# Kernel tuning notes

Hardware: AMD Instinct MI355X
Metric: run time of the kernel (lower is better)

## Reference

```python
import jax, jax.numpy as jnp
import numpy as np

B, N, DIM = 4, 2048, 1024
H, DH = 16, 64
SCALE = DH ** -0.5


def setup_inputs() -> dict:
    key = jax.random.key(0)
    k1, k2, k3, k4 = jax.random.split(key, 4)
    x = jax.random.normal(k1, (B, N, DIM), dtype=jnp.float32)
    mask = jax.random.randint(k2, (B, N, N), 0, 2, dtype=jnp.int32)
    W_qkv = jax.random.normal(k3, (DIM, 3 * H * DH), dtype=jnp.float32) * (DIM ** -0.5)
    W_out = jax.random.normal(k4, (H * DH, DIM), dtype=jnp.float32) * ((H * DH) ** -0.5)
    b_out = jnp.zeros((DIM,), dtype=jnp.float32)
    return {"x": x, "mask": mask, "W_qkv": W_qkv, "W_out": W_out, "b_out": b_out}


def reference(x, mask, W_qkv, W_out, b_out):
    # QKV projection: [b, n, 3*h*d]
    qkv = x @ W_qkv
    q, k, v = jnp.split(qkv, 3, axis=-1)
    # 'b n (h d) -> b h n d'
    def to_heads(t):
        b, n, _ = t.shape
        return t.reshape(b, n, H, DH).transpose(0, 2, 1, 3)
    q, k, v = to_heads(q), to_heads(k), to_heads(v)
    # scaled dot-product scores: [b, h, n, n]
    scores = jnp.einsum('bhnd,bhmd->bhnm', q, k) * SCALE
    scores = jnp.where(mask[:, None, :, :] == 1, -jnp.inf, scores)
    att = jax.nn.softmax(scores, axis=-1)
    out = jnp.einsum('bhnm,bhmd->bhnd', att, v)
    # 'b h n d -> b n (h d)'
    out = out.transpose(0, 2, 1, 3).reshape(x.shape[0], x.shape[1], H * DH)
    return out @ W_out + b_out
```

## Files before the change

kernel.cpp:

```cpp
#include <hip/hip_runtime.h>
#include <hip/hip_bf16.h>


typedef __attribute__((ext_vector_type(8))) short bf16x8;
typedef __attribute__((ext_vector_type(4))) float f32x4;

__device__ __forceinline__ unsigned short f2bf(float f) {
  unsigned u = __builtin_bit_cast(unsigned, f);
  u += 0x7fffu + ((u >> 16) & 1u);
  return (unsigned short)(u >> 16);
}

__device__ __forceinline__ void gload16(const void* g, void* l) {
  __builtin_amdgcn_global_load_lds(
      (const __attribute__((address_space(1))) unsigned int*)g,
      (__attribute__((address_space(3))) unsigned int*)l, 16, 0, 0);
}

__device__ __forceinline__ bf16x8 ldsw(const short* base, int row, int elem) {
  const char* p = (const char*)base + row * 128 + ((elem * 2) ^ ((row & 7) << 4));
  return *(const bf16x8*)p;
}

__global__ __launch_bounds__(256) void k_cvt(const float* __restrict__ in,
                                             unsigned short* __restrict__ out) {
  int i = (blockIdx.x * 256 + threadIdx.x) * 4;
  float4 v = *reinterpret_cast<const float4*>(in + i);
  ushort4 o;
  o.x = f2bf(v.x); o.y = f2bf(v.y); o.z = f2bf(v.z); o.w = f2bf(v.w);
  *reinterpret_cast<ushort4*>(out + i) = o;
}

__global__ __launch_bounds__(256) void k_transpose_cvt(const float* __restrict__ in,
                                                       unsigned short* __restrict__ out,
                                                       int rows, int cols) {
  __shared__ float tile[32][33];
  int tx = threadIdx.x & 31, ty = threadIdx.x >> 5;
  int c0 = blockIdx.x * 32, r0 = blockIdx.y * 32;
#pragma unroll
  for (int i = 0; i < 32; i += 8)
    tile[ty + i][tx] = in[(size_t)(r0 + ty + i) * cols + (c0 + tx)];
  __syncthreads();
#pragma unroll
  for (int i = 0; i < 32; i += 8)
    out[(size_t)(c0 + ty + i) * rows + (r0 + tx)] = f2bf(tile[tx][ty + i]);
}

__global__ __launch_bounds__(256) void k_packmask(const int* __restrict__ mask,
                                                  unsigned long long* __restrict__ pack) {
  const int row = blockIdx.x;
  const int t = threadIdx.x, w = t >> 6, lane = t & 63;
  const int* mrow = mask + (size_t)row * 2048;
#pragma unroll
  for (int it = 0; it < 8; ++it) {
    int key = it * 256 + w * 64 + lane;
    unsigned long long bal = __ballot(mrow[key] == 1);
    if (lane == 0) pack[(size_t)row * 32 + it * 4 + w] = bal;
  }
}

template <int EPI>
__global__ __launch_bounds__(256) void k_gemm(
    const unsigned short* __restrict__ A, const unsigned short* __restrict__ Bt,
    unsigned short* __restrict__ Qo, unsigned short* __restrict__ Ko,
    unsigned short* __restrict__ Vo, float* __restrict__ Co,
    const float* __restrict__ bias) {
  __shared__ __align__(16) short As[128 * 64];
  __shared__ __align__(16) short Bs[128 * 64];
  const int t = threadIdx.x;
  const int bn = blockIdx.x, bm = blockIdx.y;
  const int wid = t >> 6, lane = t & 63, g = lane >> 4, l15 = lane & 15;
  const int wr = wid >> 1, wc = wid & 1;
  f32x4 zero = {0.f, 0.f, 0.f, 0.f};
  f32x4 acc[4][4];
#pragma unroll
  for (int i = 0; i < 4; ++i)
#pragma unroll
    for (int j = 0; j < 4; ++j) acc[i][j] = zero;

  const char* Ab = (const char*)(A + (size_t)bm * 128 * 1024);
  const char* Bb = (const char*)(Bt + (size_t)bn * 128 * 1024);

  for (int k0 = 0; k0 < 2048; k0 += 128) {
#pragma unroll
    for (int q = 0; q < 4; ++q) {
      int idx = t + q * 256, r = idx >> 3, c = idx & 7;
      int sw = (c * 16) ^ ((r & 7) << 4);
      gload16(Ab + (size_t)r * 2048 + k0 + sw, (char*)As + idx * 16);
      gload16(Bb + (size_t)r * 2048 + k0 + sw, (char*)Bs + idx * 16);
    }
    asm volatile("s_waitcnt vmcnt(0)" ::: "memory");
    __syncthreads();
#pragma unroll
    for (int ks = 0; ks < 2; ++ks) {
      bf16x8 a[4], b[4];
#pragma unroll
      for (int mi = 0; mi < 4; ++mi) a[mi] = ldsw(As, wr * 64 + mi * 16 + l15, ks * 32 + g * 8);
#pragma unroll
      for (int ni = 0; ni < 4; ++ni) b[ni] = ldsw(Bs, wc * 64 + ni * 16 + l15, ks * 32 + g * 8);
#pragma unroll
      for (int mi = 0; mi < 4; ++mi)
#pragma unroll
        for (int ni = 0; ni < 4; ++ni)
          acc[mi][ni] = __builtin_amdgcn_mfma_f32_16x16x32_bf16(a[mi], b[ni], acc[mi][ni], 0, 0, 0);
    }
    __syncthreads();
  }

#pragma unroll
  for (int mi = 0; mi < 4; ++mi) {
#pragma unroll
    for (int ni = 0; ni < 4; ++ni) {
#pragma unroll
      for (int j = 0; j < 4; ++j) {
        float v = acc[mi][ni][j];
        int row = bm * 128 + wr * 64 + mi * 16 + g * 4 + j;
        int col = bn * 128 + wc * 64 + ni * 16 + l15;
        if (EPI == 0) {
          int b = row >> 11, nn = row & 2047;
          int s = col >> 10, rem = col & 1023;
          int h = rem >> 6, d = rem & 63;
          int bh = b * 16 + h;
          if (s == 0) Qo[(((size_t)bh) * 2048 + nn) * 64 + d] = f2bf(v * 0.18033688011112042f);
          else if (s == 1) Ko[(((size_t)bh) * 2048 + nn) * 64 + d] = f2bf(v);
          else Vo[(((size_t)bh) * 64 + d) * 2048 + nn] = f2bf(v);
        } else {
          Co[(size_t)row * 1024 + col] = v + bias[col];
        }
      }
    }
  }
}

__global__ __launch_bounds__(512, 5) void k_attn(
    const unsigned short* __restrict__ Q, const unsigned short* __restrict__ K,
    const unsigned short* __restrict__ Vt_g, const unsigned long long* __restrict__ pack,
    unsigned short* __restrict__ O) {
  __shared__ __align__(16) short Ks[2][64 * 64];
  __shared__ __align__(16) short Vt[2][64 * 64];
  __shared__ __align__(16) short Ps[8][16 * 72];
  const int bid0 = blockIdx.x;
  const int bid = (bid0 & 7) * 128 + (bid0 >> 3);
  const int qt = bid & 15, bh = bid >> 4;
  const int b = bh >> 4;
  const int t = threadIdx.x, wid = t >> 6, lane = t & 63, g = lane >> 4, l15 = lane & 15;
  const char* Kb = (const char*)(K + (size_t)bh * (2048 * 64));
  const char* Vb = (const char*)(Vt_g + (size_t)bh * (64 * 2048));
  const unsigned short* Qb = Q + (size_t)bh * (2048 * 64);

  {
    int r = t >> 3, c = t & 7;
    int sw = (c * 16) ^ ((r & 7) << 4);
    gload16(Kb + (size_t)r * 128 + sw, (char*)Ks[0] + t * 16);
    gload16(Vb + (size_t)r * 4096 + sw, (char*)Vt[0] + t * 16);
  }
  const int qrow = qt * 128 + wid * 16 + l15;
  bf16x8 qf0 = *reinterpret_cast<const bf16x8*>(Qb + (size_t)qrow * 64 + g * 8);
  bf16x8 qf1 = *reinterpret_cast<const bf16x8*>(Qb + (size_t)qrow * 64 + 32 + g * 8);
  asm volatile("s_waitcnt vmcnt(0)" ::: "memory");
  __syncthreads();

  f32x4 zero = {0.f, 0.f, 0.f, 0.f};
  f32x4 oacc[4];
#pragma unroll
  for (int nf = 0; nf < 4; ++nf) oacc[nf] = zero;
  float lp = 0.f;
  const unsigned long long* mrow = pack + ((size_t)b * 2048 + qrow) * 32;
  short* Pw = &Ps[wid][0];

  int cb = 0;
  for (int kt = 0; kt < 32; ++kt) {
    unsigned long long mw = mrow[kt];
    if (kt + 1 < 32) {
      int r = t >> 3, c = t & 7;
      int sw = (c * 16) ^ ((r & 7) << 4);
      gload16(Kb + (size_t)((kt + 1) * 64 + r) * 128 + sw, (char*)Ks[cb ^ 1] + t * 16);
      gload16(Vb + (size_t)r * 4096 + (kt + 1) * 128 + sw, (char*)Vt[cb ^ 1] + t * 16);
    }

    f32x4 sf[4];
#pragma unroll
    for (int nf = 0; nf < 4; ++nf) sf[nf] = zero;
    __builtin_amdgcn_s_setprio(1);
#pragma unroll
    for (int ks = 0; ks < 2; ++ks) {
      bf16x8 qk = ks ? qf1 : qf0;
#pragma unroll
      for (int nf = 0; nf < 4; ++nf) {
        bf16x8 kk = ldsw(Ks[cb], nf * 16 + l15, ks * 32 + g * 8);
        sf[nf] = __builtin_amdgcn_mfma_f32_16x16x32_bf16(kk, qk, sf[nf], 0, 0, 0);
      }
    }
    __builtin_amdgcn_s_setprio(0);

    unsigned mlo = (unsigned)mw >> (g * 4);
    unsigned mhi = (unsigned)(mw >> 32) >> (g * 4);
#pragma unroll
    for (int nf = 0; nf < 4; ++nf) {
      unsigned msrc = (nf < 2) ? mlo : mhi;
      unsigned eu[4];
#pragma unroll
      for (int j = 0; j < 4; ++j) {
        float s = sf[nf][j];
        if (msrc & (1u << ((nf & 1) * 16 + j))) s = -1e30f;
        float e = __builtin_amdgcn_exp2f(s);
        lp += e;
        eu[j] = __builtin_bit_cast(unsigned, e);
      }
      uint2 pk;
      pk.x = __builtin_amdgcn_perm(eu[1], eu[0], 0x07060302);
      pk.y = __builtin_amdgcn_perm(eu[3], eu[2], 0x07060302);
      *reinterpret_cast<uint2*>(&Pw[l15 * 72 + nf * 16 + g * 4]) = pk;
    }
    asm volatile("s_waitcnt lgkmcnt(0)" ::: "memory");
    __builtin_amdgcn_sched_barrier(0);

    __builtin_amdgcn_s_setprio(1);
#pragma unroll
    for (int ks = 0; ks < 2; ++ks) {
      bf16x8 ap = *reinterpret_cast<const bf16x8*>(&Pw[l15 * 72 + ks * 32 + g * 8]);
#pragma unroll
      for (int nf = 0; nf < 4; ++nf) {
        bf16x8 bv = ldsw(Vt[cb], nf * 16 + l15, ks * 32 + g * 8);
        oacc[nf] = __builtin_amdgcn_mfma_f32_16x16x32_bf16(ap, bv, oacc[nf], 0, 0, 0);
      }
    }
    __builtin_amdgcn_s_setprio(0);

    asm volatile("s_waitcnt vmcnt(0)" ::: "memory");
    __syncthreads();
    cb ^= 1;
  }

  float l = lp;
  l += __shfl_xor(l, 16);
  l += __shfl_xor(l, 32);
  float invl = 1.0f / l;
  float inv[4];
#pragma unroll
  for (int j = 0; j < 4; ++j) inv[j] = __shfl(invl, g * 4 + j);

  const int h = bh & 15;
#pragma unroll
  for (int nf = 0; nf < 4; ++nf) {
#pragma unroll
    for (int j = 0; j < 4; ++j) {
      int qg = qt * 128 + wid * 16 + g * 4 + j;
      int d = nf * 16 + l15;
      O[((size_t)b * 2048 + qg) * 1024 + h * 64 + d] = f2bf(oacc[nf][j] * inv[j]);
    }
  }
}

extern "C" void kernel_launch(void* const* d_in, const int* in_sizes, int n_in,
                              void* d_out, int out_size, void* d_ws, size_t ws_size,
                              hipStream_t stream) {
  (void)in_sizes; (void)n_in; (void)out_size; (void)ws_size;
  const float* x = (const float*)d_in[0];
  const int* mask = (const int*)d_in[1];
  const float* Wqkv = (const float*)d_in[2];
  const float* Wout = (const float*)d_in[3];
  const float* bout = (const float*)d_in[4];
  float* out = (float*)d_out;

  unsigned short* ws = (unsigned short*)d_ws;
  unsigned short* Xb   = ws;
  unsigned short* Wq_t = Xb + 8388608;
  unsigned short* Wo_t = Wq_t + 3145728;
  unsigned short* Qa   = Wo_t + 1048576;
  unsigned short* Ka   = Qa + 8388608;
  unsigned short* Va   = Ka + 8388608;
  unsigned short* ATT  = Va + 8388608;
  unsigned long long* MP = (unsigned long long*)(ATT + 8388608);

  k_cvt<<<8192, 256, 0, stream>>>(x, Xb);
  k_transpose_cvt<<<dim3(96, 32), 256, 0, stream>>>(Wqkv, Wq_t, 1024, 3072);
  k_transpose_cvt<<<dim3(32, 32), 256, 0, stream>>>(Wout, Wo_t, 1024, 1024);
  k_packmask<<<8192, 256, 0, stream>>>(mask, MP);
  k_gemm<0><<<dim3(24, 64), 256, 0, stream>>>(Xb, Wq_t, Qa, Ka, Va, nullptr, nullptr);
  k_attn<<<1024, 512, 0, stream>>>(Qa, Ka, Va, MP, ATT);
  k_gemm<1><<<dim3(8, 64), 256, 0, stream>>>(ATT, Wo_t, nullptr, nullptr, nullptr, out, bout);
}
```

Before: 256.3 us.

## Split attention tile into key halves, shrink swizzled P buffer, raise occupancy

The attention inner loop now handles each 64-key tile as two 32-key halves. Each half computes scores, writes the exponentiated P into a smaller XOR-swizzled per-wave LDS buffer, and immediately runs its PV MFMAs. The mask word for the next tile is prefetched alongside the K/V loads, the double-buffer loop is unrolled by two so buffer pointers are static, and launch bounds ask for 8 waves per SIMD instead of 5. The aim is lower register and LDS pressure for higher occupancy and fewer bank conflicts. The cost is an extra lgkmcnt wait and dependency point per tile, and a possible spill risk under the tighter register budget.

```diff
diff --git a/kernel.cpp b/kernel.cpp
--- a/kernel.cpp
+++ b/kernel.cpp
@@ -132,13 +132,13 @@
   }
 }
 
-__global__ __launch_bounds__(512, 5) void k_attn(
+__global__ __launch_bounds__(512, 8) void k_attn(
     const unsigned short* __restrict__ Q, const unsigned short* __restrict__ K,
     const unsigned short* __restrict__ Vt_g, const unsigned long long* __restrict__ pack,
     unsigned short* __restrict__ O) {
   __shared__ __align__(16) short Ks[2][64 * 64];
   __shared__ __align__(16) short Vt[2][64 * 64];
-  __shared__ __align__(16) short Ps[8][16 * 72];
+  __shared__ __align__(16) short Ps[8][16 * 32];
   const int bid0 = blockIdx.x;
   const int bid = (bid0 & 7) * 128 + (bid0 >> 3);
   const int qt = bid & 15, bh = bid >> 4;
@@ -148,15 +148,20 @@
   const char* Vb = (const char*)(Vt_g + (size_t)bh * (64 * 2048));
   const unsigned short* Qb = Q + (size_t)bh * (2048 * 64);
 
-  {
-    int r = t >> 3, c = t & 7;
-    int sw = (c * 16) ^ ((r & 7) << 4);
-    gload16(Kb + (size_t)r * 128 + sw, (char*)Ks[0] + t * 16);
-    gload16(Vb + (size_t)r * 4096 + sw, (char*)Vt[0] + t * 16);
-  }
+  const int sr = t >> 3, sc = t & 7;
+  const int sw_src = (sc * 16) ^ ((sr & 7) << 4);
+  char* PwB = (char*)&Ps[wid][0];
+  const int ps_rd  = (l15 * 64 + g * 16) ^ ((l15 & 7) << 4);
+  const int ps_wr0 = (l15 * 64 + g * 8) ^ ((l15 & 7) << 4);
+  const int ps_wr1 = (l15 * 64 + 32 + g * 8) ^ ((l15 & 7) << 4);
+
+  gload16(Kb + (size_t)sr * 128 + sw_src, (char*)&Ks[0][0] + t * 16);
+  gload16(Vb + (size_t)sr * 4096 + sw_src, (char*)&Vt[0][0] + t * 16);
   const int qrow = qt * 128 + wid * 16 + l15;
   bf16x8 qf0 = *reinterpret_cast<const bf16x8*>(Qb + (size_t)qrow * 64 + g * 8);
   bf16x8 qf1 = *reinterpret_cast<const bf16x8*>(Qb + (size_t)qrow * 64 + 32 + g * 8);
+  const unsigned long long* mrow = pack + ((size_t)b * 2048 + qrow) * 32;
+  unsigned long long mwc = mrow[0];
   asm volatile("s_waitcnt vmcnt(0)" ::: "memory");
   __syncthreads();
 
@@ -165,71 +170,67 @@
 #pragma unroll
   for (int nf = 0; nf < 4; ++nf) oacc[nf] = zero;
   float lp = 0.f;
-  const unsigned long long* mrow = pack + ((size_t)b * 2048 + qrow) * 32;
-  short* Pw = &Ps[wid][0];
-
-  int cb = 0;
-  for (int kt = 0; kt < 32; ++kt) {
-    unsigned long long mw = mrow[kt];
+
+  auto tile = [&](int kt, const short* KsC, const short* VtC,
+                  char* KsN, char* VtN) {
+    unsigned long long mwn = 0;
     if (kt + 1 < 32) {
-      int r = t >> 3, c = t & 7;
-      int sw = (c * 16) ^ ((r & 7) << 4);
-      gload16(Kb + (size_t)((kt + 1) * 64 + r) * 128 + sw, (char*)Ks[cb ^ 1] + t * 16);
-      gload16(Vb + (size_t)r * 4096 + (kt + 1) * 128 + sw, (char*)Vt[cb ^ 1] + t * 16);
-    }
-
-    f32x4 sf[4];
-#pragma unroll
-    for (int nf = 0; nf < 4; ++nf) sf[nf] = zero;
-    __builtin_amdgcn_s_setprio(1);
-#pragma unroll
-    for (int ks = 0; ks < 2; ++ks) {
-      bf16x8 qk = ks ? qf1 : qf0;
+      gload16(Kb + (size_t)((kt + 1) * 64 + sr) * 128 + sw_src, KsN + t * 16);
+      gload16(Vb + (size_t)sr * 4096 + (kt + 1) * 128 + sw_src, VtN + t * 16);
+      mwn = mrow[kt + 1];
+    }
+    unsigned mlo = (unsigned)mwc >> (g * 4);
+    unsigned mhi = (unsigned)(mwc >> 32) >> (g * 4);
+#pragma unroll
+    for (int kh = 0; kh < 2; ++kh) {
+      f32x4 sf[2] = {zero, zero};
+      __builtin_amdgcn_s_setprio(1);
+#pragma unroll
+      for (int ds = 0; ds < 2; ++ds) {
+        bf16x8 qk = ds ? qf1 : qf0;
+#pragma unroll
+        for (int nf2 = 0; nf2 < 2; ++nf2) {
+          bf16x8 kk = ldsw(KsC, (kh * 2 + nf2) * 16 + l15, ds * 32 + g * 8);
+          sf[nf2] = __builtin_amdgcn_mfma_f32_16x16x32_bf16(kk, qk, sf[nf2], 0, 0, 0);
+        }
+      }
+      __builtin_amdgcn_s_setprio(0);
+      unsigned msrc = kh ? mhi : mlo;
+#pragma unroll
+      for (int nf2 = 0; nf2 < 2; ++nf2) {
+        unsigned eu[4];
+#pragma unroll
+        for (int j = 0; j < 4; ++j) {
+          float s = sf[nf2][j];
+          if (msrc & (1u << (nf2 * 16 + j))) s = -1e30f;
+          float e = __builtin_amdgcn_exp2f(s);
+          lp += e;
+          eu[j] = __builtin_bit_cast(unsigned, e);
+        }
+        uint2 pk;
+        pk.x = __builtin_amdgcn_perm(eu[1], eu[0], 0x07060302);
+        pk.y = __builtin_amdgcn_perm(eu[3], eu[2], 0x07060302);
+        *reinterpret_cast<uint2*>(PwB + (nf2 ? ps_wr1 : ps_wr0)) = pk;
+      }
+      asm volatile("s_waitcnt lgkmcnt(0)" ::: "memory");
+      __builtin_amdgcn_sched_barrier(0);
+      bf16x8 ap = *reinterpret_cast<const bf16x8*>(PwB + ps_rd);
+      __builtin_amdgcn_s_setprio(1);
 #pragma unroll
       for (int nf = 0; nf < 4; ++nf) {
-        bf16x8 kk = ldsw(Ks[cb], nf * 16 + l15, ks * 32 + g * 8);
-        sf[nf] = __builtin_amdgcn_mfma_f32_16x16x32_bf16(kk, qk, sf[nf], 0, 0, 0);
-      }
-    }
-    __builtin_amdgcn_s_setprio(0);
-
-    unsigned mlo = (unsigned)mw >> (g * 4);
-    unsigned mhi = (unsigned)(mw >> 32) >> (g * 4);
-#pragma unroll
-    for (int nf = 0; nf < 4; ++nf) {
-      unsigned msrc = (nf < 2) ? mlo : mhi;
-      unsigned eu[4];
-#pragma unroll
-      for (int j = 0; j < 4; ++j) {
-        float s = sf[nf][j];
-        if (msrc & (1u << ((nf & 1) * 16 + j))) s = -1e30f;
-        float e = __builtin_amdgcn_exp2f(s);
-        lp += e;
-        eu[j] = __builtin_bit_cast(unsigned, e);
-      }
-      uint2 pk;
-      pk.x = __builtin_amdgcn_perm(eu[1], eu[0], 0x07060302);
-      pk.y = __builtin_amdgcn_perm(eu[3], eu[2], 0x07060302);
-      *reinterpret_cast<uint2*>(&Pw[l15 * 72 + nf * 16 + g * 4]) = pk;
-    }
-    asm volatile("s_waitcnt lgkmcnt(0)" ::: "memory");
-    __builtin_amdgcn_sched_barrier(0);
-
-    __builtin_amdgcn_s_setprio(1);
-#pragma unroll
-    for (int ks = 0; ks < 2; ++ks) {
-      bf16x8 ap = *reinterpret_cast<const bf16x8*>(&Pw[l15 * 72 + ks * 32 + g * 8]);
-#pragma unroll
-      for (int nf = 0; nf < 4; ++nf) {
-        bf16x8 bv = ldsw(Vt[cb], nf * 16 + l15, ks * 32 + g * 8);
+        bf16x8 bv = ldsw(VtC, nf * 16 + l15, kh * 32 + g * 8);
         oacc[nf] = __builtin_amdgcn_mfma_f32_16x16x32_bf16(ap, bv, oacc[nf], 0, 0, 0);
       }
-    }
-    __builtin_amdgcn_s_setprio(0);
-
+      __builtin_amdgcn_s_setprio(0);
+    }
     asm volatile("s_waitcnt vmcnt(0)" ::: "memory");
     __syncthreads();
-    cb ^= 1;
+    mwc = mwn;
+  };
+
+  for (int kt = 0; kt < 32; kt += 2) {
+    tile(kt,     &Ks[0][0], &Vt[0][0], (char*)&Ks[1][0], (char*)&Vt[1][0]);
+    tile(kt + 1, &Ks[1][0], &Vt[1][0], (char*)&Ks[0][0], (char*)&Vt[0][0]);
   }
 
   float l = lp;
```

Measured after the change: 352.7 us. 1.38x slower.
